# Kernel tuning notes

Measured on AMD Instinct MI355X. Metric: run time of the kernel, lower is better.

The kernel has to match this reference:

```python
import jax, jax.numpy as jnp
import numpy as np

WS = 7  # window size
NH = 8  # num heads


def _relative_position_index(ws):
    coords = np.stack(np.meshgrid(np.arange(ws), np.arange(ws), indexing='ij'), axis=0)
    flat = coords.reshape(2, -1)                       # [2, ws*ws]
    rel = flat[:, :, None] - flat[:, None, :]          # [2, N, N]
    rel = rel.transpose(1, 2, 0)                       # [N, N, 2]
    xx = (rel[:, :, 0] + ws - 1) * (2 * ws - 1)
    yy = rel[:, :, 1] + ws - 1
    return jnp.asarray(xx + yy, dtype=jnp.int32)       # [N, N]


def setup_inputs() -> dict:
    key = jax.random.key(0)
    ks = jax.random.split(key, 6)
    B_, N, C = 4096, WS * WS, 256
    return {
        'x': jax.random.normal(ks[0], (B_, N, C), dtype=jnp.float32),
        'qkv_w': jax.random.normal(ks[1], (C, 3 * C), dtype=jnp.float32) * 0.02,
        'qkv_b': jax.random.normal(ks[2], (3 * C,), dtype=jnp.float32) * 0.02,
        'rpb_table': jax.random.normal(ks[3], ((2 * WS - 1) ** 2, NH), dtype=jnp.float32) * 0.02,
        'proj_w': jax.random.normal(ks[4], (C, C), dtype=jnp.float32) * 0.02,
        'proj_b': jax.random.normal(ks[5], (C,), dtype=jnp.float32) * 0.02,
    }


def reference(x, qkv_w, qkv_b, rpb_table, proj_w, proj_b):
    B_, N, C = x.shape
    D = C // NH
    scale = D ** -0.5
    rpi = _relative_position_index(WS)                  # [N, N] int

    qkv = x @ qkv_w + qkv_b                             # [B, N, 3C]
    qkv = qkv.reshape(B_, N, 3, NH, D).transpose(2, 0, 3, 1, 4)
    q, k, v = qkv[0], qkv[1], qkv[2]                    # each [B, H, N, D]

    attn = jnp.einsum('bhnd,bhmd->bhnm', q * scale, k)  # [B, H, N, N]
    bias = rpb_table[rpi.reshape(-1)].reshape(N, N, NH).transpose(2, 0, 1)
    attn = jax.nn.softmax(attn + bias[None], axis=-1)

    out = jnp.einsum('bhnm,bhmd->bhnd', attn, v)        # [B, H, N, D]
    out = out.transpose(0, 2, 1, 3).reshape(B_, N, C)
    return out @ proj_w + proj_b
```

## Files before the change

kernel.cpp:

```cpp
#include <hip/hip_runtime.h>
#include <stdint.h>


typedef __attribute__((ext_vector_type(8))) short bf16x8;
typedef __attribute__((ext_vector_type(4))) float f32x4;

__device__ __forceinline__ unsigned short f2bf(float f) {
    unsigned u = __float_as_uint(f);
    u += 0x7fffu + ((u >> 16) & 1u);
    return (unsigned short)(u >> 16);
}
__device__ __forceinline__ unsigned pk2(float a, float b) {
    return (unsigned)f2bf(a) | ((unsigned)f2bf(b) << 16);
}

__global__ void k_prep(const float* __restrict__ qkv_w, const float* __restrict__ proj_w,
                       short* __restrict__ Wqkv_t, short* __restrict__ Wproj_t) {
    int tid = blockIdx.x * 256 + threadIdx.x;
    if (tid < 196608) {
        int nn = tid >> 8, kk = tid & 255;
        Wqkv_t[tid] = (short)f2bf(qkv_w[kk * 768 + nn]);
    } else {
        int t2 = tid - 196608;
        int nn = t2 >> 8, kk = t2 & 255;
        Wproj_t[t2] = (short)f2bf(proj_w[kk * 256 + nn]);
    }
}

#define XS_OFF 0
#define AO_OFF 0
#define SW_OFF 16384

#define QKV_PASS(P, ACC)                                                          \
    {                                                                             \
        const short* wb = Wq + (size_t)((P) * 256 + w * 32 + l15) * 256 + g * 8;  \
        _Pragma("unroll")                                                         \
        for (int ks = 0; ks < 8; ks++) {                                          \
            bf16x8 af0 = *(const bf16x8*)(wb + ks * 32);                          \
            bf16x8 af1 = *(const bf16x8*)(wb + 4096 + ks * 32);                   \
            int xsl = (((ks << 2) + g) ^ (l15 & 7)) << 3;                         \
            _Pragma("unroll")                                                     \
            for (int j = 0; j < 4; j++) {                                         \
                bf16x8 bfj = *(const bf16x8*)&smem[XS_OFF + (j * 16 + l15) * 256 + xsl]; \
                ACC[0][j] = __builtin_amdgcn_mfma_f32_16x16x32_bf16(af0, bfj, ACC[0][j], 0, 0, 0); \
                ACC[1][j] = __builtin_amdgcn_mfma_f32_16x16x32_bf16(af1, bfj, ACC[1][j], 0, 0, 0); \
            }                                                                     \
        }                                                                         \
    }

__global__ __launch_bounds__(512, 4) void k_fused(
        const float* __restrict__ x, const short* __restrict__ Wq,
        const short* __restrict__ Wp, const float* __restrict__ qkv_b,
        const float* __restrict__ rpb, const float* __restrict__ proj_b,
        float* __restrict__ out) {
    __shared__ __align__(16) short smem[34816];
    __shared__ float rpbs[1352];

    const int b = blockIdx.x;
    const int t = threadIdx.x;
    const int w = t >> 6, lane = t & 63;
    const int l15 = lane & 15, g = lane >> 4;
    const int cs8 = (l15 >> 1) & 3;
    const int swz = (g ^ cs8) << 3;

    f32x4 zero = {0.f, 0.f, 0.f, 0.f};

    for (int i = t; i < 1352; i += 512) rpbs[(i & 7) * 169 + (i >> 3)] = rpb[i];
    #pragma unroll
    for (int i = 0; i < 4; i++) {
        int cid = t + i * 512;
        int tok = cid >> 5, c = cid & 31;
        uint4 w4 = make_uint4(0u, 0u, 0u, 0u);
        if (tok < 49) {
            const float4* s = (const float4*)(x + ((size_t)b * 49 + tok) * 256 + c * 8);
            float4 f0 = s[0], f1 = s[1];
            w4 = make_uint4(pk2(f0.x, f0.y), pk2(f0.z, f0.w),
                            pk2(f1.x, f1.y), pk2(f1.z, f1.w));
        }
        *(uint4*)&smem[XS_OFF + tok * 256 + ((c ^ (tok & 7)) << 3)] = w4;
    }
    __syncthreads();

    short* SW = &smem[SW_OFF + w * 2304];
    const int d0a = g * 4;
    const int d0b = 16 + g * 4;
    const int sda = (((d0a >> 3) ^ cs8) << 3) + (d0a & 7);
    const int sdb = (((d0b >> 3) ^ cs8) << 3) + (d0b & 7);

    bf16x8 qb4[4], ka[4], va[2][2];

    {
        f32x4 aq[2][4];
        #pragma unroll
        for (int i = 0; i < 2; i++)
            #pragma unroll
            for (int j = 0; j < 4; j++) aq[i][j] = zero;
        QKV_PASS(0, aq)
        #pragma unroll
        for (int it = 0; it < 2; it++) {
            float4 bv = *(const float4*)&qkv_b[w * 32 + it * 16 + d0a];
            int sd = it ? sdb : sda;
            #pragma unroll
            for (int j = 0; j < 4; j++) {
                f32x4 a = aq[it][j];
                unsigned* dst = (unsigned*)&SW[(j * 16 + l15) * 32 + sd];
                dst[0] = pk2(a[0] + bv.x, a[1] + bv.y);
                dst[1] = pk2(a[2] + bv.z, a[3] + bv.w);
            }
        }
        #pragma unroll
        for (int nt = 0; nt < 4; nt++)
            qb4[nt] = *(const bf16x8*)&SW[(nt * 16 + l15) * 32 + swz];
    }
    {
        f32x4 ak[2][4];
        #pragma unroll
        for (int i = 0; i < 2; i++)
            #pragma unroll
            for (int j = 0; j < 4; j++) ak[i][j] = zero;
        QKV_PASS(1, ak)
        #pragma unroll
        for (int it = 0; it < 2; it++) {
            float4 bv = *(const float4*)&qkv_b[256 + w * 32 + it * 16 + d0a];
            int sd = it ? sdb : sda;
            #pragma unroll
            for (int j = 0; j < 4; j++) {
                f32x4 a = ak[it][j];
                unsigned* dst = (unsigned*)&SW[(j * 16 + l15) * 32 + sd];
                dst[0] = pk2(a[0] + bv.x, a[1] + bv.y);
                dst[1] = pk2(a[2] + bv.z, a[3] + bv.w);
            }
        }
        #pragma unroll
        for (int mt = 0; mt < 4; mt++)
            ka[mt] = *(const bf16x8*)&SW[(mt * 16 + l15) * 32 + swz];
    }
    {
        f32x4 av[2][4];
        #pragma unroll
        for (int i = 0; i < 2; i++)
            #pragma unroll
            for (int j = 0; j < 4; j++) av[i][j] = zero;
        QKV_PASS(2, av)
        #pragma unroll
        for (int it = 0; it < 2; it++) {
            float4 bv = *(const float4*)&qkv_b[512 + w * 32 + it * 16 + d0a];
            int d0 = it * 16 + d0a;
            #pragma unroll
            for (int j = 0; j < 4; j++) {
                int tok = j * 16 + l15;
                f32x4 a = av[it][j];
                SW[(d0 + 0) * 72 + tok] = (short)f2bf(a[0] + bv.x);
                SW[(d0 + 1) * 72 + tok] = (short)f2bf(a[1] + bv.y);
                SW[(d0 + 2) * 72 + tok] = (short)f2bf(a[2] + bv.z);
                SW[(d0 + 3) * 72 + tok] = (short)f2bf(a[3] + bv.w);
            }
        }
        #pragma unroll
        for (int dt = 0; dt < 2; dt++)
            #pragma unroll
            for (int kk = 0; kk < 2; kk++)
                va[dt][kk] = *(const bf16x8*)&SW[(dt * 16 + l15) * 72 + kk * 32 + g * 8];
    }
    __syncthreads();

    {
        const int h = w;
        short* Plw = SW;
        short* AOw = &smem[AO_OFF + h * 2048];
        const float* rh = &rpbs[h * 169];
        const float scale = 0.17677669529663687f;

        #pragma unroll
        for (int nt = 0; nt < 4; nt++) {
            f32x4 s4[4];
            #pragma unroll
            for (int mt = 0; mt < 4; mt++)
                s4[mt] = __builtin_amdgcn_mfma_f32_16x16x32_bf16(ka[mt], qb4[nt], zero, 0, 0, 0);
            int n = nt * 16 + l15;
            int ni = n / 7;
            int an = 13 * ni + (n - 7 * ni) + 84;
            #pragma unroll
            for (int mt = 0; mt < 4; mt++)
                #pragma unroll
                for (int r = 0; r < 4; r++) {
                    int m = mt * 16 + g * 4 + r;
                    int mi = m / 7;
                    int idx = an - (13 * mi + (m - 7 * mi));
                    idx = idx < 0 ? 0 : (idx > 168 ? 168 : idx);
                    float val = s4[mt][r] * scale + rh[idx];
                    s4[mt][r] = (m < 49) ? val : -1e30f;
                }
            float tmax = -1e30f;
            #pragma unroll
            for (int mt = 0; mt < 4; mt++)
                #pragma unroll
                for (int r = 0; r < 4; r++) tmax = fmaxf(tmax, s4[mt][r]);
            tmax = fmaxf(tmax, __shfl_xor(tmax, 16));
            tmax = fmaxf(tmax, __shfl_xor(tmax, 32));
            float rsum = 0.f;
            #pragma unroll
            for (int mt = 0; mt < 4; mt++)
                #pragma unroll
                for (int r = 0; r < 4; r++) {
                    float e = __expf(s4[mt][r] - tmax);
                    s4[mt][r] = e;
                    rsum += e;
                }
            rsum += __shfl_xor(rsum, 16);
            rsum += __shfl_xor(rsum, 32);

            #pragma unroll
            for (int mt = 0; mt < 4; mt++) {
                unsigned* dst = (unsigned*)&Plw[l15 * 72 + mt * 16 + g * 4];
                dst[0] = pk2(s4[mt][0], s4[mt][1]);
                dst[1] = pk2(s4[mt][2], s4[mt][3]);
            }
            bf16x8 pb0 = *(const bf16x8*)&Plw[l15 * 72 + g * 8];
            bf16x8 pb1 = *(const bf16x8*)&Plw[l15 * 72 + 32 + g * 8];
            f32x4 o0 = __builtin_amdgcn_mfma_f32_16x16x32_bf16(va[0][0], pb0, zero, 0, 0, 0);
            o0 = __builtin_amdgcn_mfma_f32_16x16x32_bf16(va[0][1], pb1, o0, 0, 0, 0);
            f32x4 o1 = __builtin_amdgcn_mfma_f32_16x16x32_bf16(va[1][0], pb0, zero, 0, 0, 0);
            o1 = __builtin_amdgcn_mfma_f32_16x16x32_bf16(va[1][1], pb1, o1, 0, 0, 0);
            float inv = 1.f / rsum;
            {
                unsigned* dst = (unsigned*)&AOw[n * 32 + sda];
                dst[0] = pk2(o0[0] * inv, o0[1] * inv);
                dst[1] = pk2(o0[2] * inv, o0[3] * inv);
            }
            {
                unsigned* dst = (unsigned*)&AOw[n * 32 + sdb];
                dst[0] = pk2(o1[0] * inv, o1[1] * inv);
                dst[1] = pk2(o1[2] * inv, o1[3] * inv);
            }
        }
    }
    __syncthreads();

    {
        f32x4 acc2[2][4];
        #pragma unroll
        for (int i = 0; i < 2; i++)
            #pragma unroll
            for (int j = 0; j < 4; j++) acc2[i][j] = zero;

        const short* pbase = Wp + (size_t)(w * 32 + l15) * 256 + g * 8;
        #pragma unroll
        for (int ks = 0; ks < 8; ks++) {
            bf16x8 af2[2], bf2[4];
            af2[0] = *(const bf16x8*)(pbase + ks * 32);
            af2[1] = *(const bf16x8*)(pbase + 4096 + ks * 32);
            #pragma unroll
            for (int j = 0; j < 4; j++)
                bf2[j] = *(const bf16x8*)&smem[AO_OFF + ks * 2048 + (j * 16 + l15) * 32 + swz];
            #pragma unroll
            for (int i = 0; i < 2; i++)
                #pragma unroll
                for (int j = 0; j < 4; j++)
                    acc2[i][j] = __builtin_amdgcn_mfma_f32_16x16x32_bf16(
                        af2[i], bf2[j], acc2[i][j], 0, 0, 0);
        }
        #pragma unroll
        for (int it = 0; it < 2; it++) {
            int fo = w * 32 + it * 16 + g * 4;
            float4 bv = *(const float4*)&proj_b[fo];
            #pragma unroll
            for (int j = 0; j < 4; j++) {
                int tok = j * 16 + l15;
                if (tok < 49) {
                    f32x4 a = acc2[it][j];
                    float4 val = make_float4(a[0] + bv.x, a[1] + bv.y,
                                             a[2] + bv.z, a[3] + bv.w);
                    *(float4*)&out[((size_t)b * 49 + tok) * 256 + fo] = val;
                }
            }
        }
    }
}

extern "C" void kernel_launch(void* const* d_in, const int* in_sizes, int n_in,
                              void* d_out, int out_size, void* d_ws, size_t ws_size,
                              hipStream_t stream) {
    const float* x      = (const float*)d_in[0];
    const float* qkv_w  = (const float*)d_in[1];
    const float* qkv_b  = (const float*)d_in[2];
    const float* rpb    = (const float*)d_in[3];
    const float* proj_w = (const float*)d_in[4];
    const float* proj_b = (const float*)d_in[5];
    float* out = (float*)d_out;

    short* Wqkv_t  = (short*)d_ws;
    short* Wproj_t = Wqkv_t + 768 * 256;
    if (ws_size < 524288ull) return;

    k_prep<<<1024, 256, 0, stream>>>(qkv_w, proj_w, Wqkv_t, Wproj_t);
    k_fused<<<4096, 512, 0, stream>>>(x, Wqkv_t, Wproj_t, qkv_b, rpb, proj_b, out);
}
```

Baseline: 583.2 us.

## Precompute dense bias table, tile weight transpose, prefetch weight fragments

The prep kernel now transposes the weights through shared-memory tiles, which coalesces the global reads, and also expands the relative-position bias into a dense [H,64,64] table in workspace. The fused kernel reads bias values straight from global memory as float4 vectors, replacing the per-element div/mod index math and the shared-memory bias staging. Weight fragments in the QKV and projection GEMM loops are software-prefetched one k-step ahead. The cost is extra global traffic for the bias table, 128KB read by every block though it should stay cached, plus higher register pressure.

```diff
diff --git a/kernel.cpp b/kernel.cpp
--- a/kernel.cpp
+++ b/kernel.cpp
@@ -1,29 +1,65 @@
 #include <hip/hip_runtime.h>
+#include <hip/hip_bf16.h>
 #include <stdint.h>
 
 
 typedef __attribute__((ext_vector_type(8))) short bf16x8;
 typedef __attribute__((ext_vector_type(4))) float f32x4;
 
-__device__ __forceinline__ unsigned short f2bf(float f) {
-    unsigned u = __float_as_uint(f);
-    u += 0x7fffu + ((u >> 16) & 1u);
-    return (unsigned short)(u >> 16);
+__device__ __forceinline__ unsigned short f2bfu(float f) {
+    __hip_bfloat16 h = __float2bfloat16(f);
+    return *reinterpret_cast<unsigned short*>(&h);
 }
 __device__ __forceinline__ unsigned pk2(float a, float b) {
-    return (unsigned)f2bf(a) | ((unsigned)f2bf(b) << 16);
-}
-
-__global__ void k_prep(const float* __restrict__ qkv_w, const float* __restrict__ proj_w,
-                       short* __restrict__ Wqkv_t, short* __restrict__ Wproj_t) {
-    int tid = blockIdx.x * 256 + threadIdx.x;
-    if (tid < 196608) {
-        int nn = tid >> 8, kk = tid & 255;
-        Wqkv_t[tid] = (short)f2bf(qkv_w[kk * 768 + nn]);
+    return (unsigned)f2bfu(a) | ((unsigned)f2bfu(b) << 16);
+}
+
+__global__ __launch_bounds__(256) void k_prep(const float* __restrict__ qkv_w,
+        const float* __restrict__ proj_w, const float* __restrict__ rpb,
+        short* __restrict__ Wcat, float* __restrict__ RB) {
+    int blk = blockIdx.x;
+    int t = threadIdx.x;
+    if (blk < 16) {
+        __shared__ float ft[64 * 65];
+        int n0 = blk * 64;
+        const float* src;
+        int stride, c0;
+        if (blk < 12) { src = qkv_w;  stride = 768; c0 = n0; }
+        else          { src = proj_w; stride = 256; c0 = n0 - 768; }
+        for (int k0 = 0; k0 < 256; k0 += 64) {
+            __syncthreads();
+            #pragma unroll
+            for (int i = 0; i < 4; i++) {
+                int idx = i * 256 + t;
+                int kk = idx >> 4, c4 = (idx & 15) * 4;
+                float4 v = *(const float4*)(src + (size_t)(k0 + kk) * stride + c0 + c4);
+                float* d = &ft[kk * 65 + c4];
+                d[0] = v.x; d[1] = v.y; d[2] = v.z; d[3] = v.w;
+            }
+            __syncthreads();
+            #pragma unroll
+            for (int j = 0; j < 2; j++) {
+                int idx = j * 256 + t;
+                int nn = idx >> 3, c8 = (idx & 7) * 8;
+                unsigned u0 = pk2(ft[(c8 + 0) * 65 + nn], ft[(c8 + 1) * 65 + nn]);
+                unsigned u1 = pk2(ft[(c8 + 2) * 65 + nn], ft[(c8 + 3) * 65 + nn]);
+                unsigned u2 = pk2(ft[(c8 + 4) * 65 + nn], ft[(c8 + 5) * 65 + nn]);
+                unsigned u3 = pk2(ft[(c8 + 6) * 65 + nn], ft[(c8 + 7) * 65 + nn]);
+                *(uint4*)&Wcat[(size_t)(n0 + nn) * 256 + k0 + c8] =
+                    make_uint4(u0, u1, u2, u3);
+            }
+        }
     } else {
-        int t2 = tid - 196608;
-        int nn = t2 >> 8, kk = t2 & 255;
-        Wproj_t[t2] = (short)f2bf(proj_w[kk * 256 + nn]);
+        int flat = (blk - 16) * 256 + t;
+        int h = flat >> 12, n = (flat >> 6) & 63, m = flat & 63;
+        float v = 0.f;
+        if (n < 49 && m < 49) {
+            int ni = n / 7, nj = n - 7 * ni;
+            int mi = m / 7, mj = m - 7 * mi;
+            int idx = (ni - mi + 6) * 13 + (nj - mj + 6);
+            v = rpb[idx * 8 + h];
+        }
+        RB[flat] = v;
     }
 }
 
@@ -34,27 +70,32 @@
 #define QKV_PASS(P, ACC)                                                          \
     {                                                                             \
         const short* wb = Wq + (size_t)((P) * 256 + w * 32 + l15) * 256 + g * 8;  \
+        bf16x8 c0 = *(const bf16x8*)(wb);                                         \
+        bf16x8 c1 = *(const bf16x8*)(wb + 4096);                                  \
         _Pragma("unroll")                                                         \
         for (int ks = 0; ks < 8; ks++) {                                          \
-            bf16x8 af0 = *(const bf16x8*)(wb + ks * 32);                          \
-            bf16x8 af1 = *(const bf16x8*)(wb + 4096 + ks * 32);                   \
+            bf16x8 p0, p1;                                                        \
+            if (ks < 7) {                                                         \
+                p0 = *(const bf16x8*)(wb + (ks + 1) * 32);                        \
+                p1 = *(const bf16x8*)(wb + 4096 + (ks + 1) * 32);                 \
+            }                                                                     \
             int xsl = (((ks << 2) + g) ^ (l15 & 7)) << 3;                         \
             _Pragma("unroll")                                                     \
             for (int j = 0; j < 4; j++) {                                         \
                 bf16x8 bfj = *(const bf16x8*)&smem[XS_OFF + (j * 16 + l15) * 256 + xsl]; \
-                ACC[0][j] = __builtin_amdgcn_mfma_f32_16x16x32_bf16(af0, bfj, ACC[0][j], 0, 0, 0); \
-                ACC[1][j] = __builtin_amdgcn_mfma_f32_16x16x32_bf16(af1, bfj, ACC[1][j], 0, 0, 0); \
+                ACC[0][j] = __builtin_amdgcn_mfma_f32_16x16x32_bf16(c0, bfj, ACC[0][j], 0, 0, 0); \
+                ACC[1][j] = __builtin_amdgcn_mfma_f32_16x16x32_bf16(c1, bfj, ACC[1][j], 0, 0, 0); \
             }                                                                     \
+            if (ks < 7) { c0 = p0; c1 = p1; }                                     \
         }                                                                         \
     }
 
 __global__ __launch_bounds__(512, 4) void k_fused(
         const float* __restrict__ x, const short* __restrict__ Wq,
         const short* __restrict__ Wp, const float* __restrict__ qkv_b,
-        const float* __restrict__ rpb, const float* __restrict__ proj_b,
+        const float* __restrict__ RB, const float* __restrict__ proj_b,
         float* __restrict__ out) {
     __shared__ __align__(16) short smem[34816];
-    __shared__ float rpbs[1352];
 
     const int b = blockIdx.x;
     const int t = threadIdx.x;
@@ -65,7 +106,6 @@
 
     f32x4 zero = {0.f, 0.f, 0.f, 0.f};
 
-    for (int i = t; i < 1352; i += 512) rpbs[(i & 7) * 169 + (i >> 3)] = rpb[i];
     #pragma unroll
     for (int i = 0; i < 4; i++) {
         int cid = t + i * 512;
@@ -150,10 +190,10 @@
             for (int j = 0; j < 4; j++) {
                 int tok = j * 16 + l15;
                 f32x4 a = av[it][j];
-                SW[(d0 + 0) * 72 + tok] = (short)f2bf(a[0] + bv.x);
-                SW[(d0 + 1) * 72 + tok] = (short)f2bf(a[1] + bv.y);
-                SW[(d0 + 2) * 72 + tok] = (short)f2bf(a[2] + bv.z);
-                SW[(d0 + 3) * 72 + tok] = (short)f2bf(a[3] + bv.w);
+                SW[(d0 + 0) * 72 + tok] = (short)f2bfu(a[0] + bv.x);
+                SW[(d0 + 1) * 72 + tok] = (short)f2bfu(a[1] + bv.y);
+                SW[(d0 + 2) * 72 + tok] = (short)f2bfu(a[2] + bv.z);
+                SW[(d0 + 3) * 72 + tok] = (short)f2bfu(a[3] + bv.w);
             }
         }
         #pragma unroll
@@ -168,27 +208,25 @@
         const int h = w;
         short* Plw = SW;
         short* AOw = &smem[AO_OFF + h * 2048];
-        const float* rh = &rpbs[h * 169];
         const float scale = 0.17677669529663687f;
 
         #pragma unroll
         for (int nt = 0; nt < 4; nt++) {
+            int n = nt * 16 + l15;
+            const float* RBp = RB + (((h << 6) + n) << 6) + (g << 2);
+            f32x4 bb[4];
+            #pragma unroll
+            for (int mt = 0; mt < 4; mt++) bb[mt] = *(const f32x4*)(RBp + mt * 16);
             f32x4 s4[4];
             #pragma unroll
             for (int mt = 0; mt < 4; mt++)
                 s4[mt] = __builtin_amdgcn_mfma_f32_16x16x32_bf16(ka[mt], qb4[nt], zero, 0, 0, 0);
-            int n = nt * 16 + l15;
-            int ni = n / 7;
-            int an = 13 * ni + (n - 7 * ni) + 84;
             #pragma unroll
             for (int mt = 0; mt < 4; mt++)
                 #pragma unroll
                 for (int r = 0; r < 4; r++) {
                     int m = mt * 16 + g * 4 + r;
-                    int mi = m / 7;
-                    int idx = an - (13 * mi + (m - 7 * mi));
-                    idx = idx < 0 ? 0 : (idx > 168 ? 168 : idx);
-                    float val = s4[mt][r] * scale + rh[idx];
+                    float val = s4[mt][r] * scale + bb[mt][r];
                     s4[mt][r] = (m < 49) ? val : -1e30f;
                 }
             float tmax = -1e30f;
@@ -245,20 +283,22 @@
             for (int j = 0; j < 4; j++) acc2[i][j] = zero;
 
         const short* pbase = Wp + (size_t)(w * 32 + l15) * 256 + g * 8;
+        bf16x8 c0 = *(const bf16x8*)(pbase);
+        bf16x8 c1 = *(const bf16x8*)(pbase + 4096);
         #pragma unroll
         for (int ks = 0; ks < 8; ks++) {
-            bf16x8 af2[2], bf2[4];
-            af2[0] = *(const bf16x8*)(pbase + ks * 32);
-            af2[1] = *(const bf16x8*)(pbase + 4096 + ks * 32);
-            #pragma unroll
-            for (int j = 0; j < 4; j++)
-                bf2[j] = *(const bf16x8*)&smem[AO_OFF + ks * 2048 + (j * 16 + l15) * 32 + swz];
-            #pragma unroll
-            for (int i = 0; i < 2; i++)
-                #pragma unroll
-                for (int j = 0; j < 4; j++)
-                    acc2[i][j] = __builtin_amdgcn_mfma_f32_16x16x32_bf16(
-                        af2[i], bf2[j], acc2[i][j], 0, 0, 0);
+            bf16x8 p0, p1;
+            if (ks < 7) {
+                p0 = *(const bf16x8*)(pbase + (ks + 1) * 32);
+                p1 = *(const bf16x8*)(pbase + 4096 + (ks + 1) * 32);
+            }
+            #pragma unroll
+            for (int j = 0; j < 4; j++) {
+                bf16x8 bf2 = *(const bf16x8*)&smem[AO_OFF + ks * 2048 + (j * 16 + l15) * 32 + swz];
+                acc2[0][j] = __builtin_amdgcn_mfma_f32_16x16x32_bf16(c0, bf2, acc2[0][j], 0, 0, 0);
+                acc2[1][j] = __builtin_amdgcn_mfma_f32_16x16x32_bf16(c1, bf2, acc2[1][j], 0, 0, 0);
+            }
+            if (ks < 7) { c0 = p0; c1 = p1; }
         }
         #pragma unroll
         for (int it = 0; it < 2; it++) {
@@ -289,10 +329,10 @@
     const float* proj_b = (const float*)d_in[5];
     float* out = (float*)d_out;
 
-    short* Wqkv_t  = (short*)d_ws;
-    short* Wproj_t = Wqkv_t + 768 * 256;
-    if (ws_size < 524288ull) return;
-
-    k_prep<<<1024, 256, 0, stream>>>(qkv_w, proj_w, Wqkv_t, Wproj_t);
-    k_fused<<<4096, 512, 0, stream>>>(x, Wqkv_t, Wproj_t, qkv_b, rpb, proj_b, out);
-}
+    short* Wcat = (short*)d_ws;
+    float* RB   = (float*)(Wcat + 1024 * 256);
+    if (ws_size < 655360ull) return;
+
+    k_prep<<<144, 256, 0, stream>>>(qkv_w, proj_w, rpb, Wcat, RB);
+    k_fused<<<4096, 512, 0, stream>>>(x, Wcat, Wcat + 768 * 256, qkv_b, RB, proj_b, out);
+}
```

Result: slower. 606.6 us (+4.0%).
